# Performance work log

Hardware: AMD Instinct MI355X
Metric: run time of the kernel (lower is better)

Reference implementation:

```python
import jax, jax.numpy as jnp
import numpy as np

B, T, D = 2, 1024, 1024
U = 50257   # units (vocab)
S = 8192    # negatives sampled


def setup_inputs() -> dict:
    key = jax.random.key(0)
    k1, k2, k3, k4, k5 = jax.random.split(key, 5)
    logits = jax.random.normal(k1, (B, T, D), dtype=jnp.float32)
    kernel = jax.random.normal(k2, (U, D), dtype=jnp.float32) * 0.02
    bias = jax.random.normal(k3, (U,), dtype=jnp.float32) * 0.01
    targets = jax.random.randint(k4, (B, T), 0, U, dtype=jnp.int32)
    sampled = jax.random.randint(k5, (S,), 0, U, dtype=jnp.int32)
    return {"logits": logits, "kernel": kernel, "bias": bias,
            "targets": targets, "sampled": sampled}


def _log_uniform_logq(ids, num_classes):
    # log of log-uniform (Zipfian) sampling probability, as in
    # tf.random.log_uniform_candidate_sampler
    idf = ids.astype(jnp.float32)
    return jnp.log(jnp.log1p(1.0 / (idf + 1.0)) / jnp.log(float(num_classes + 1)))


def reference(logits, kernel, bias, targets, sampled):
    num_classes = kernel.shape[0]
    num_sampled = sampled.shape[0]
    x = logits.reshape(-1, logits.shape[-1])      # [N, D]
    t = targets.reshape(-1)                        # [N]

    # Full-softmax output probabilities (layer's returned tensor)
    full_logits = x @ kernel.T + bias              # [N, U]
    probs = jax.nn.softmax(full_logits, axis=-1)

    # Sampled softmax training loss (tf.nn.sampled_softmax_loss math)
    log_s = jnp.log(jnp.float32(num_sampled))
    true_w = kernel[t]                             # [N, D] gather
    true_b = bias[t]
    true_logits = jnp.sum(x * true_w, axis=-1) + true_b \
        - (log_s + _log_uniform_logq(t, num_classes))          # [N]

    samp_w = kernel[sampled]                       # [S, D] gather
    samp_b = bias[sampled]
    samp_logits = x @ samp_w.T + samp_b \
        - (log_s + _log_uniform_logq(sampled, num_classes))    # [N, S]

    # remove accidental hits: sampled negative equals the true class
    acc = t[:, None] == sampled[None, :]
    samp_logits = jnp.where(acc, jnp.float32(-1e9), samp_logits)

    all_logits = jnp.concatenate([true_logits[:, None], samp_logits], axis=1)
    # cross entropy with label index 0 (the true class slot)
    per_token = jax.nn.logsumexp(all_logits, axis=1) - all_logits[:, 0]
    loss = jnp.mean(per_token)  # weights all ones -> SUM_OVER_BATCH_SIZE

    return probs.reshape(targets.shape + (num_classes,)), loss
```

## Files before the change

### kernel.cpp

```cpp
#include <hip/hip_runtime.h>
#include <hip/hip_bf16.h>
#include <stdint.h>

#define N_ROWS 2048
#define DK 1024
#define NU 50257
#define NS 8192

typedef __bf16 bf16x8 __attribute__((ext_vector_type(8)));
typedef float f32x4 __attribute__((ext_vector_type(4)));
typedef float vf4 __attribute__((ext_vector_type(4)));
typedef unsigned vu2 __attribute__((ext_vector_type(2)));
typedef unsigned vu4 __attribute__((ext_vector_type(4)));

__device__ __forceinline__ unsigned short f2bf_rne(float f) {
  union { float f; unsigned u; } v; v.f = f;
  unsigned u = v.u;
  return (unsigned short)((u + 0x7FFFu + ((u >> 16) & 1u)) >> 16);
}
__device__ __forceinline__ unsigned pack2(float lo, float hi) {
  return (unsigned)f2bf_rne(lo) | ((unsigned)f2bf_rne(hi) << 16);
}

__global__ void cvt_f32_bf16(const float* __restrict__ in,
                             unsigned short* __restrict__ out, unsigned n) {
  unsigned i = (blockIdx.x * 256u + threadIdx.x) * 8u;
  if (i >= n) return;
  const vf4* p = (const vf4*)(in + i);
  vf4 a = __builtin_nontemporal_load(p);
  vf4 b = __builtin_nontemporal_load(p + 1);
  vu4 o;
  o.x = pack2(a.x, a.y); o.y = pack2(a.z, a.w);
  o.z = pack2(b.x, b.y); o.w = pack2(b.z, b.w);
  *(vu4*)(out + i) = o;
}

__global__ void gather_sampled(const float* __restrict__ kern,
                               const float* __restrict__ bias,
                               const int* __restrict__ sampled,
                               unsigned short* __restrict__ sw,
                               float* __restrict__ adj) {
  int j = blockIdx.x;
  int s = sampled[j];
  const float* src = kern + (size_t)s * DK;
  unsigned short* dst = sw + (size_t)j * DK;
  int c = threadIdx.x * 4;
  vf4 v = __builtin_nontemporal_load((const vf4*)(src + c));
  vu2 o; o.x = pack2(v.x, v.y); o.y = pack2(v.z, v.w);
  *(vu2*)(dst + c) = o;
  if (threadIdx.x == 0) {
    float lq = logf(log1pf(1.0f / ((float)s + 1.0f))) - logf(logf((float)(NU + 1)));
    adj[j] = bias[s] - (logf((float)NS) + lq);
  }
}

__global__ void true_logits_k(const float* __restrict__ x, const float* __restrict__ kern,
                              const float* __restrict__ bias, const int* __restrict__ targets,
                              float* __restrict__ true_logit, float* __restrict__ loss_acc) {
  int row = blockIdx.x * 4 + (threadIdx.x >> 6);
  int lane = threadIdx.x & 63;
  int t = targets[row];
  const float* xr = x + (size_t)row * DK;
  const float* wr = kern + (size_t)t * DK;
  float s = 0.f;
  #pragma unroll
  for (int it = 0; it < 4; ++it) {
    int c = lane * 4 + it * 256;
    float4 a = *(const float4*)(xr + c);
    float4 b = *(const float4*)(wr + c);
    s += a.x * b.x + a.y * b.y + a.z * b.z + a.w * b.w;
  }
  #pragma unroll
  for (int off = 32; off > 0; off >>= 1) s += __shfl_xor(s, off, 64);
  if (lane == 0) {
    float lq = logf(log1pf(1.0f / ((float)t + 1.0f))) - logf(logf((float)(NU + 1)));
    float tl = s + bias[t] - (logf((float)NS) + lq);
    true_logit[row] = tl;
    atomicAdd(&loss_acc[row], __expf(tl));
  }
}

__global__ __launch_bounds__(256) void gemm_probs(
    const unsigned short* __restrict__ A,
    const unsigned short* __restrict__ Bm,
    const float* __restrict__ bias,
    float* __restrict__ out, float* __restrict__ row_sum) {
  __shared__ alignas(16) unsigned char smem[32 * 132 * 4];
  unsigned short* As = (unsigned short*)smem;
  unsigned short* Bs = (unsigned short*)(smem + 8192);
  float* ot = (float*)smem;

  const int tid = threadIdx.x;
  const int wave = tid >> 6, lane = tid & 63;
  const int bid = blockIdx.x;
  const int sb = (bid & 7) * 786 + (bid >> 3);
  const int rb = (sb & 15) << 7;
  const int cb = (sb >> 4) << 7;
  const int wm = wave & 1, wn = wave >> 1;
  const int q = lane >> 4, l15 = lane & 15;
  const int srow = lane >> 2, scol = lane & 3;

  f32x4 acc[4][4] = {};

  const int seg0 = wave * 2;
  const unsigned short* ga0 = A + (size_t)(rb + seg0 * 16 + srow) * DK + scol * 8;
  const unsigned short* ga1 = ga0 + (size_t)16 * DK;
  int bu0 = cb + seg0 * 16 + srow;       if (bu0 > NU - 1) bu0 = NU - 1;
  int bu1 = cb + (seg0 + 1) * 16 + srow; if (bu1 > NU - 1) bu1 = NU - 1;
  const unsigned short* gb0 = Bm + (size_t)bu0 * DK + scol * 8;
  const unsigned short* gb1 = Bm + (size_t)bu1 * DK + scol * 8;
  unsigned short* la0 = As + (seg0) * 512;
  unsigned short* la1 = As + (seg0 + 1) * 512;
  unsigned short* lb0 = Bs + (seg0) * 512;
  unsigned short* lb1 = Bs + (seg0 + 1) * 512;

  for (int kb = 0; kb < DK; kb += 32) {
    __builtin_amdgcn_global_load_lds((__attribute__((address_space(1))) void*)(ga0 + kb),
                                     (__attribute__((address_space(3))) void*)la0, 16, 0, 0);
    __builtin_amdgcn_global_load_lds((__attribute__((address_space(1))) void*)(ga1 + kb),
                                     (__attribute__((address_space(3))) void*)la1, 16, 0, 0);
    __builtin_amdgcn_global_load_lds((__attribute__((address_space(1))) void*)(gb0 + kb),
                                     (__attribute__((address_space(3))) void*)lb0, 16, 0, 0);
    __builtin_amdgcn_global_load_lds((__attribute__((address_space(1))) void*)(gb1 + kb),
                                     (__attribute__((address_space(3))) void*)lb1, 16, 0, 0);
    __syncthreads();
    bf16x8 af[4], bfr[4];
    #pragma unroll
    for (int mi = 0; mi < 4; ++mi)
      af[mi] = *(const bf16x8*)&As[(wm * 64 + mi * 16 + l15) * 32 + q * 8];
    #pragma unroll
    for (int ni = 0; ni < 4; ++ni)
      bfr[ni] = *(const bf16x8*)&Bs[(wn * 64 + ni * 16 + l15) * 32 + q * 8];
    #pragma unroll
    for (int mi = 0; mi < 4; ++mi)
      #pragma unroll
      for (int ni = 0; ni < 4; ++ni)
        acc[mi][ni] = __builtin_amdgcn_mfma_f32_16x16x32_bf16(af[mi], bfr[ni], acc[mi][ni], 0, 0, 0);
    __syncthreads();
  }

  const bool full_panel = (cb + 128 <= NU);
  #pragma unroll
  for (int mi = 0; mi < 4; ++mi) {
    #pragma unroll
    for (int ni = 0; ni < 4; ++ni) {
      int col = cb + wn * 64 + ni * 16 + l15;
      int bcol = col < NU ? col : NU - 1;
      float bv = bias[bcol];
      f32x4 c = acc[mi][ni];
      #pragma unroll
      for (int r = 0; r < 4; ++r)
        ot[(wm * 16 + q * 4 + r) * 132 + wn * 64 + ni * 16 + l15] = __expf(c[r] + bv);
    }
    __syncthreads();
    {
      int lr = tid >> 3;
      int sub = tid & 7;
      int grow = rb + (lr >> 4) * 64 + mi * 16 + (lr & 15);
      float* gout = out + (size_t)grow * NU + cb;
      const float* lrow = ot + lr * 132;
      float sum = 0.f;
      if (full_panel) {
        #pragma unroll
        for (int p = 0; p < 4; ++p) {
          int c = p * 32 + sub * 4;
          vf4 v = *(const vf4*)(lrow + c);
          sum += v.x + v.y + v.z + v.w;
          __builtin_nontemporal_store(v, (vf4*)(gout + c));
        }
      } else {
        #pragma unroll
        for (int p = 0; p < 4; ++p) {
          int c = p * 32 + sub * 4;
          #pragma unroll
          for (int e = 0; e < 4; ++e) {
            if (cb + c + e < NU) {
              float v = lrow[c + e];
              sum += v;
              __builtin_nontemporal_store(v, gout + c + e);
            }
          }
        }
      }
      sum += __shfl_xor(sum, 1, 64);
      sum += __shfl_xor(sum, 2, 64);
      sum += __shfl_xor(sum, 4, 64);
      if (sub == 0) atomicAdd(&row_sum[grow], sum);
    }
    __syncthreads();
  }
}

__global__ __launch_bounds__(256) void gemm_sampled(
    const unsigned short* __restrict__ A, const unsigned short* __restrict__ SW,
    const float* __restrict__ adj, const int* __restrict__ sampled,
    const int* __restrict__ targets, float* __restrict__ loss_acc) {
  __shared__ alignas(16) unsigned short As[128 * 32];
  __shared__ alignas(16) unsigned short Bs[128 * 32];
  const int tid = threadIdx.x;
  const int wave = tid >> 6, lane = tid & 63;
  const int bid = blockIdx.x;
  const int sb = (bid & 7) * 128 + (bid >> 3);
  const int rb = (sb & 15) << 7;
  const int cb = (sb >> 4) << 7;
  const int wm = wave & 1, wn = wave >> 1;
  const int q = lane >> 4, l15 = lane & 15;
  const int srow = lane >> 2, scol = lane & 3;

  f32x4 acc[4][4] = {};

  const int seg0 = wave * 2;
  const unsigned short* ga0 = A + (size_t)(rb + seg0 * 16 + srow) * DK + scol * 8;
  const unsigned short* ga1 = ga0 + (size_t)16 * DK;
  const unsigned short* gb0 = SW + (size_t)(cb + seg0 * 16 + srow) * DK + scol * 8;
  const unsigned short* gb1 = gb0 + (size_t)16 * DK;
  unsigned short* la0 = &As[(seg0) * 512];
  unsigned short* la1 = &As[(seg0 + 1) * 512];
  unsigned short* lb0 = &Bs[(seg0) * 512];
  unsigned short* lb1 = &Bs[(seg0 + 1) * 512];

  for (int kb = 0; kb < DK; kb += 32) {
    __builtin_amdgcn_global_load_lds((__attribute__((address_space(1))) void*)(ga0 + kb),
                                     (__attribute__((address_space(3))) void*)la0, 16, 0, 0);
    __builtin_amdgcn_global_load_lds((__attribute__((address_space(1))) void*)(ga1 + kb),
                                     (__attribute__((address_space(3))) void*)la1, 16, 0, 0);
    __builtin_amdgcn_global_load_lds((__attribute__((address_space(1))) void*)(gb0 + kb),
                                     (__attribute__((address_space(3))) void*)lb0, 16, 0, 0);
    __builtin_amdgcn_global_load_lds((__attribute__((address_space(1))) void*)(gb1 + kb),
                                     (__attribute__((address_space(3))) void*)lb1, 16, 0, 0);
    __syncthreads();
    bf16x8 af[4], bfr[4];
    #pragma unroll
    for (int mi = 0; mi < 4; ++mi)
      af[mi] = *(const bf16x8*)&As[(wm * 64 + mi * 16 + l15) * 32 + q * 8];
    #pragma unroll
    for (int ni = 0; ni < 4; ++ni)
      bfr[ni] = *(const bf16x8*)&Bs[(wn * 64 + ni * 16 + l15) * 32 + q * 8];
    #pragma unroll
    for (int mi = 0; mi < 4; ++mi)
      #pragma unroll
      for (int ni = 0; ni < 4; ++ni)
        acc[mi][ni] = __builtin_amdgcn_mfma_f32_16x16x32_bf16(af[mi], bfr[ni], acc[mi][ni], 0, 0, 0);
    __syncthreads();
  }

  #pragma unroll
  for (int mi = 0; mi < 4; ++mi) {
    int row0 = rb + wm * 64 + mi * 16 + q * 4;
    int t0 = targets[row0], t1 = targets[row0 + 1], t2 = targets[row0 + 2], t3 = targets[row0 + 3];
    float rs[4] = {0.f, 0.f, 0.f, 0.f};
    #pragma unroll
    for (int ni = 0; ni < 4; ++ni) {
      int col = cb + wn * 64 + ni * 16 + l15;
      float av = adj[col];
      int sid = sampled[col];
      f32x4 c = acc[mi][ni];
      rs[0] += (sid == t0) ? 0.f : __expf(c[0] + av);
      rs[1] += (sid == t1) ? 0.f : __expf(c[1] + av);
      rs[2] += (sid == t2) ? 0.f : __expf(c[2] + av);
      rs[3] += (sid == t3) ? 0.f : __expf(c[3] + av);
    }
    #pragma unroll
    for (int r = 0; r < 4; ++r) {
      float v = rs[r];
      v += __shfl_xor(v, 1, 64);
      v += __shfl_xor(v, 2, 64);
      v += __shfl_xor(v, 4, 64);
      v += __shfl_xor(v, 8, 64);
      if (l15 == 0) atomicAdd(&loss_acc[row0 + r], v);
    }
  }
}

__global__ void prep_inv(const float* __restrict__ row_sum, float* __restrict__ inv) {
  int i = blockIdx.x * 256 + threadIdx.x;
  if (i < N_ROWS) inv[i] = 1.0f / row_sum[i];
}

__global__ void scale_probs(float* __restrict__ out, const float* __restrict__ inv, unsigned n4) {
  unsigned i = blockIdx.x * 256u + threadIdx.x;
  if (i >= n4) return;
  constexpr unsigned long long MAGIC = ((1ull << 45) + 50256ull) / 50257ull;
  vf4 v = __builtin_nontemporal_load((const vf4*)out + i);
  unsigned long long base = (unsigned long long)i * 4ull;
  unsigned r0 = (unsigned)((base * MAGIC) >> 45);
  unsigned r1 = (unsigned)(((base + 1) * MAGIC) >> 45);
  unsigned r2 = (unsigned)(((base + 2) * MAGIC) >> 45);
  unsigned r3 = (unsigned)(((base + 3) * MAGIC) >> 45);
  v.x *= inv[r0]; v.y *= inv[r1]; v.z *= inv[r2]; v.w *= inv[r3];
  __builtin_nontemporal_store(v, (vf4*)out + i);
}

__global__ void finalize_loss(const float* __restrict__ loss_acc,
                              const float* __restrict__ true_logit,
                              float* __restrict__ loss_out) {
  __shared__ float red[256];
  float s = 0.f;
  for (int i = threadIdx.x; i < N_ROWS; i += 256)
    s += logf(loss_acc[i]) - true_logit[i];
  red[threadIdx.x] = s;
  __syncthreads();
  for (int off = 128; off > 0; off >>= 1) {
    if (threadIdx.x < off) red[threadIdx.x] += red[threadIdx.x + off];
    __syncthreads();
  }
  if (threadIdx.x == 0) loss_out[0] = red[0] / (float)N_ROWS;
}

extern "C" void kernel_launch(void* const* d_in, const int* in_sizes, int n_in,
                              void* d_out, int out_size, void* d_ws, size_t ws_size,
                              hipStream_t stream) {
  const float* x = (const float*)d_in[0];
  const float* kern = (const float*)d_in[1];
  const float* bias = (const float*)d_in[2];
  const int* targets = (const int*)d_in[3];
  const int* sampled = (const int*)d_in[4];
  float* out = (float*)d_out;

  char* ws = (char*)d_ws;
  size_t off = 0;
  unsigned short* kbf = (unsigned short*)(ws + off); off += (size_t)NU * DK * 2;
  unsigned short* xbf = (unsigned short*)(ws + off); off += (size_t)N_ROWS * DK * 2;
  unsigned short* swbf = (unsigned short*)(ws + off); off += (size_t)NS * DK * 2;
  float* adj = (float*)(ws + off); off += (size_t)NS * 4;
  float* row_sum = (float*)(ws + off); off += (size_t)N_ROWS * 4;
  float* inv_rs = (float*)(ws + off); off += (size_t)N_ROWS * 4;
  float* loss_acc = (float*)(ws + off); off += (size_t)N_ROWS * 4;
  float* true_l = (float*)(ws + off); off += (size_t)N_ROWS * 4;

  hipMemsetAsync(row_sum, 0, N_ROWS * 4, stream);
  hipMemsetAsync(loss_acc, 0, N_ROWS * 4, stream);

  {
    unsigned n = NU * DK;
    cvt_f32_bf16<<<(n / 8 + 255) / 256, 256, 0, stream>>>(kern, kbf, n);
  }
  {
    unsigned n = N_ROWS * DK;
    cvt_f32_bf16<<<(n / 8 + 255) / 256, 256, 0, stream>>>(x, xbf, n);
  }
  gather_sampled<<<NS, 256, 0, stream>>>(kern, bias, sampled, swbf, adj);
  true_logits_k<<<N_ROWS / 4, 256, 0, stream>>>(x, kern, bias, targets, true_l, loss_acc);

  gemm_probs<<<dim3(6288), 256, 0, stream>>>(xbf, kbf, bias, out, row_sum);

  gemm_sampled<<<dim3(1024), 256, 0, stream>>>(xbf, swbf, adj, sampled, targets, loss_acc);

  prep_inv<<<(N_ROWS + 255) / 256, 256, 0, stream>>>(row_sum, inv_rs);

  {
    unsigned n4 = (unsigned)(((size_t)N_ROWS * NU) / 4);
    scale_probs<<<(n4 + 255u) / 256u, 256, 0, stream>>>(out, inv_rs, n4);
  }
  finalize_loss<<<1, 256, 0, stream>>>(loss_acc, true_l, out + (size_t)N_ROWS * NU);
}
```

Measured before the change: 1.031 ms.

## Gather sampled rows from bf16 kernel in-GEMM, align prob stores, row-wise scaling

```diff
diff --git a/kernel.cpp b/kernel.cpp
--- a/kernel.cpp
+++ b/kernel.cpp
@@ -35,20 +35,12 @@
   *(vu4*)(out + i) = o;
 }
 
-__global__ void gather_sampled(const float* __restrict__ kern,
-                               const float* __restrict__ bias,
-                               const int* __restrict__ sampled,
-                               unsigned short* __restrict__ sw,
-                               float* __restrict__ adj) {
-  int j = blockIdx.x;
-  int s = sampled[j];
-  const float* src = kern + (size_t)s * DK;
-  unsigned short* dst = sw + (size_t)j * DK;
-  int c = threadIdx.x * 4;
-  vf4 v = __builtin_nontemporal_load((const vf4*)(src + c));
-  vu2 o; o.x = pack2(v.x, v.y); o.y = pack2(v.z, v.w);
-  *(vu2*)(dst + c) = o;
-  if (threadIdx.x == 0) {
+__global__ void compute_adj(const float* __restrict__ bias,
+                            const int* __restrict__ sampled,
+                            float* __restrict__ adj) {
+  int j = blockIdx.x * 256 + threadIdx.x;
+  if (j < NS) {
+    int s = sampled[j];
     float lq = logf(log1pf(1.0f / ((float)s + 1.0f))) - logf(logf((float)(NU + 1)));
     adj[j] = bias[s] - (logf((float)NS) + lq);
   }
@@ -157,16 +149,64 @@
       int lr = tid >> 3;
       int sub = tid & 7;
       int grow = rb + (lr >> 4) * 64 + mi * 16 + (lr & 15);
-      float* gout = out + (size_t)grow * NU + cb;
+      size_t base = (size_t)grow * NU + cb;
+      float* gout = out + base;
       const float* lrow = ot + lr * 132;
       float sum = 0.f;
       if (full_panel) {
-        #pragma unroll
-        for (int p = 0; p < 4; ++p) {
-          int c = p * 32 + sub * 4;
-          vf4 v = *(const vf4*)(lrow + c);
-          sum += v.x + v.y + v.z + v.w;
-          __builtin_nontemporal_store(v, (vf4*)(gout + c));
+        int c0 = sub * 16;
+        vf4 v0 = *(const vf4*)(lrow + c0);
+        vf4 v1 = *(const vf4*)(lrow + c0 + 4);
+        vf4 v2 = *(const vf4*)(lrow + c0 + 8);
+        vf4 v3 = *(const vf4*)(lrow + c0 + 12);
+        sum = v0.x + v0.y + v0.z + v0.w + v1.x + v1.y + v1.z + v1.w
+            + v2.x + v2.y + v2.z + v2.w + v3.x + v3.y + v3.z + v3.w;
+        float* g = gout + c0;
+        int mis = (int)((4 - (base & 3)) & 3);
+        vf4 t;
+        switch (mis) {
+          case 0:
+            __builtin_nontemporal_store(v0, (vf4*)g);
+            __builtin_nontemporal_store(v1, (vf4*)(g + 4));
+            __builtin_nontemporal_store(v2, (vf4*)(g + 8));
+            __builtin_nontemporal_store(v3, (vf4*)(g + 12));
+            break;
+          case 1:
+            __builtin_nontemporal_store(v0.x, g);
+            t.x = v0.y; t.y = v0.z; t.z = v0.w; t.w = v1.x;
+            __builtin_nontemporal_store(t, (vf4*)(g + 1));
+            t.x = v1.y; t.y = v1.z; t.z = v1.w; t.w = v2.x;
+            __builtin_nontemporal_store(t, (vf4*)(g + 5));
+            t.x = v2.y; t.y = v2.z; t.z = v2.w; t.w = v3.x;
+            __builtin_nontemporal_store(t, (vf4*)(g + 9));
+            __builtin_nontemporal_store(v3.y, g + 13);
+            __builtin_nontemporal_store(v3.z, g + 14);
+            __builtin_nontemporal_store(v3.w, g + 15);
+            break;
+          case 2:
+            __builtin_nontemporal_store(v0.x, g);
+            __builtin_nontemporal_store(v0.y, g + 1);
+            t.x = v0.z; t.y = v0.w; t.z = v1.x; t.w = v1.y;
+            __builtin_nontemporal_store(t, (vf4*)(g + 2));
+            t.x = v1.z; t.y = v1.w; t.z = v2.x; t.w = v2.y;
+            __builtin_nontemporal_store(t, (vf4*)(g + 6));
+            t.x = v2.z; t.y = v2.w; t.z = v3.x; t.w = v3.y;
+            __builtin_nontemporal_store(t, (vf4*)(g + 10));
+            __builtin_nontemporal_store(v3.z, g + 14);
+            __builtin_nontemporal_store(v3.w, g + 15);
+            break;
+          default:
+            __builtin_nontemporal_store(v0.x, g);
+            __builtin_nontemporal_store(v0.y, g + 1);
+            __builtin_nontemporal_store(v0.z, g + 2);
+            t.x = v0.w; t.y = v1.x; t.z = v1.y; t.w = v1.z;
+            __builtin_nontemporal_store(t, (vf4*)(g + 3));
+            t.x = v1.w; t.y = v2.x; t.z = v2.y; t.w = v2.z;
+            __builtin_nontemporal_store(t, (vf4*)(g + 7));
+            t.x = v2.w; t.y = v3.x; t.z = v3.y; t.w = v3.z;
+            __builtin_nontemporal_store(t, (vf4*)(g + 11));
+            __builtin_nontemporal_store(v3.w, g + 15);
+            break;
         }
       } else {
         #pragma unroll
@@ -192,7 +232,7 @@
 }
 
 __global__ __launch_bounds__(256) void gemm_sampled(
-    const unsigned short* __restrict__ A, const unsigned short* __restrict__ SW,
+    const unsigned short* __restrict__ A, const unsigned short* __restrict__ Kb,
     const float* __restrict__ adj, const int* __restrict__ sampled,
     const int* __restrict__ targets, float* __restrict__ loss_acc) {
   __shared__ alignas(16) unsigned short As[128 * 32];
@@ -212,8 +252,10 @@
   const int seg0 = wave * 2;
   const unsigned short* ga0 = A + (size_t)(rb + seg0 * 16 + srow) * DK + scol * 8;
   const unsigned short* ga1 = ga0 + (size_t)16 * DK;
-  const unsigned short* gb0 = SW + (size_t)(cb + seg0 * 16 + srow) * DK + scol * 8;
-  const unsigned short* gb1 = gb0 + (size_t)16 * DK;
+  int s0 = sampled[cb + seg0 * 16 + srow];
+  int s1 = sampled[cb + (seg0 + 1) * 16 + srow];
+  const unsigned short* gb0 = Kb + (size_t)s0 * DK + scol * 8;
+  const unsigned short* gb1 = Kb + (size_t)s1 * DK + scol * 8;
   unsigned short* la0 = &As[(seg0) * 512];
   unsigned short* la1 = &As[(seg0 + 1) * 512];
   unsigned short* lb0 = &Bs[(seg0) * 512];
@@ -272,23 +314,25 @@
   }
 }
 
-__global__ void prep_inv(const float* __restrict__ row_sum, float* __restrict__ inv) {
-  int i = blockIdx.x * 256 + threadIdx.x;
-  if (i < N_ROWS) inv[i] = 1.0f / row_sum[i];
-}
-
-__global__ void scale_probs(float* __restrict__ out, const float* __restrict__ inv, unsigned n4) {
-  unsigned i = blockIdx.x * 256u + threadIdx.x;
-  if (i >= n4) return;
-  constexpr unsigned long long MAGIC = ((1ull << 45) + 50256ull) / 50257ull;
-  vf4 v = __builtin_nontemporal_load((const vf4*)out + i);
-  unsigned long long base = (unsigned long long)i * 4ull;
-  unsigned r0 = (unsigned)((base * MAGIC) >> 45);
-  unsigned r1 = (unsigned)(((base + 1) * MAGIC) >> 45);
-  unsigned r2 = (unsigned)(((base + 2) * MAGIC) >> 45);
-  unsigned r3 = (unsigned)(((base + 3) * MAGIC) >> 45);
-  v.x *= inv[r0]; v.y *= inv[r1]; v.z *= inv[r2]; v.w *= inv[r3];
-  __builtin_nontemporal_store(v, (vf4*)out + i);
+__global__ __launch_bounds__(256) void scale_probs_rows(float* __restrict__ out,
+                                                        const float* __restrict__ row_sum) {
+  int row = blockIdx.x;
+  size_t base = (size_t)row * NU;
+  float inv = 1.0f / row_sum[row];
+  float* p = out + base;
+  int mis = (int)((4 - (base & 3)) & 3);
+  int t = threadIdx.x;
+  if (t < mis) p[t] *= inv;
+  int nb = (NU - mis) >> 2;
+  for (int j = t; j < nb; j += 256) {
+    vf4* q = (vf4*)(p + mis + 4 * j);
+    vf4 v = __builtin_nontemporal_load(q);
+    v.x *= inv; v.y *= inv; v.z *= inv; v.w *= inv;
+    __builtin_nontemporal_store(v, q);
+  }
+  int done = mis + 4 * nb;
+  int rem = NU - done;
+  if (t < rem) p[done + t] *= inv;
 }
 
 __global__ void finalize_loss(const float* __restrict__ loss_acc,
@@ -321,10 +365,8 @@
   size_t off = 0;
   unsigned short* kbf = (unsigned short*)(ws + off); off += (size_t)NU * DK * 2;
   unsigned short* xbf = (unsigned short*)(ws + off); off += (size_t)N_ROWS * DK * 2;
-  unsigned short* swbf = (unsigned short*)(ws + off); off += (size_t)NS * DK * 2;
   float* adj = (float*)(ws + off); off += (size_t)NS * 4;
   float* row_sum = (float*)(ws + off); off += (size_t)N_ROWS * 4;
-  float* inv_rs = (float*)(ws + off); off += (size_t)N_ROWS * 4;
   float* loss_acc = (float*)(ws + off); off += (size_t)N_ROWS * 4;
   float* true_l = (float*)(ws + off); off += (size_t)N_ROWS * 4;
 
@@ -339,18 +381,14 @@
     unsigned n = N_ROWS * DK;
     cvt_f32_bf16<<<(n / 8 + 255) / 256, 256, 0, stream>>>(x, xbf, n);
   }
-  gather_sampled<<<NS, 256, 0, stream>>>(kern, bias, sampled, swbf, adj);
+  compute_adj<<<(NS + 255) / 256, 256, 0, stream>>>(bias, sampled, adj);
   true_logits_k<<<N_ROWS / 4, 256, 0, stream>>>(x, kern, bias, targets, true_l, loss_acc);
 
   gemm_probs<<<dim3(6288), 256, 0, stream>>>(xbf, kbf, bias, out, row_sum);
 
-  gemm_sampled<<<dim3(1024), 256, 0, stream>>>(xbf, swbf, adj, sampled, targets, loss_acc);
-
-  prep_inv<<<(N_ROWS + 255) / 256, 256, 0, stream>>>(row_sum, inv_rs);
-
-  {
-    unsigned n4 = (unsigned)(((size_t)N_ROWS * NU) / 4);
-    scale_probs<<<(n4 + 255u) / 256u, 256, 0, stream>>>(out, inv_rs, n4);
-  }
+  gemm_sampled<<<dim3(1024), 256, 0, stream>>>(xbf, kbf, adj, sampled, targets, loss_acc);
+
+  scale_probs_rows<<<N_ROWS, 256, 0, stream>>>(out, row_sum);
+
   finalize_loss<<<1, 256, 0, stream>>>(loss_acc, true_l, out + (size_t)N_ROWS * NU);
 }
```

Result: slower. 1.144 ms (+10.9%).

## Replace row-sum atomics with per-panel partials and row-wise scaling pass

Applied to the files above, without the earlier changes.

```diff
diff --git a/kernel.cpp b/kernel.cpp
--- a/kernel.cpp
+++ b/kernel.cpp
@@ -6,6 +6,7 @@
 #define DK 1024
 #define NU 50257
 #define NS 8192
+#define NPAN 393
 
 typedef __bf16 bf16x8 __attribute__((ext_vector_type(8)));
 typedef float f32x4 __attribute__((ext_vector_type(4)));
@@ -84,7 +85,7 @@
     const unsigned short* __restrict__ A,
     const unsigned short* __restrict__ Bm,
     const float* __restrict__ bias,
-    float* __restrict__ out, float* __restrict__ row_sum) {
+    float* __restrict__ out, float* __restrict__ part) {
   __shared__ alignas(16) unsigned char smem[32 * 132 * 4];
   unsigned short* As = (unsigned short*)smem;
   unsigned short* Bs = (unsigned short*)(smem + 8192);
@@ -95,7 +96,8 @@
   const int bid = blockIdx.x;
   const int sb = (bid & 7) * 786 + (bid >> 3);
   const int rb = (sb & 15) << 7;
-  const int cb = (sb >> 4) << 7;
+  const int panel = sb >> 4;
+  const int cb = panel << 7;
   const int wm = wave & 1, wn = wave >> 1;
   const int q = lane >> 4, l15 = lane & 15;
   const int srow = lane >> 2, scol = lane & 3;
@@ -166,7 +168,7 @@
           int c = p * 32 + sub * 4;
           vf4 v = *(const vf4*)(lrow + c);
           sum += v.x + v.y + v.z + v.w;
-          __builtin_nontemporal_store(v, (vf4*)(gout + c));
+          __builtin_memcpy(gout + c, &v, 16);
         }
       } else {
         #pragma unroll
@@ -177,7 +179,7 @@
             if (cb + c + e < NU) {
               float v = lrow[c + e];
               sum += v;
-              __builtin_nontemporal_store(v, gout + c + e);
+              gout[c + e] = v;
             }
           }
         }
@@ -185,7 +187,7 @@
       sum += __shfl_xor(sum, 1, 64);
       sum += __shfl_xor(sum, 2, 64);
       sum += __shfl_xor(sum, 4, 64);
-      if (sub == 0) atomicAdd(&row_sum[grow], sum);
+      if (sub == 0) part[(size_t)grow * NPAN + panel] = sum;
     }
     __syncthreads();
   }
@@ -272,23 +274,38 @@
   }
 }
 
-__global__ void prep_inv(const float* __restrict__ row_sum, float* __restrict__ inv) {
-  int i = blockIdx.x * 256 + threadIdx.x;
-  if (i < N_ROWS) inv[i] = 1.0f / row_sum[i];
-}
-
-__global__ void scale_probs(float* __restrict__ out, const float* __restrict__ inv, unsigned n4) {
-  unsigned i = blockIdx.x * 256u + threadIdx.x;
-  if (i >= n4) return;
-  constexpr unsigned long long MAGIC = ((1ull << 45) + 50256ull) / 50257ull;
-  vf4 v = __builtin_nontemporal_load((const vf4*)out + i);
-  unsigned long long base = (unsigned long long)i * 4ull;
-  unsigned r0 = (unsigned)((base * MAGIC) >> 45);
-  unsigned r1 = (unsigned)(((base + 1) * MAGIC) >> 45);
-  unsigned r2 = (unsigned)(((base + 2) * MAGIC) >> 45);
-  unsigned r3 = (unsigned)(((base + 3) * MAGIC) >> 45);
-  v.x *= inv[r0]; v.y *= inv[r1]; v.z *= inv[r2]; v.w *= inv[r3];
-  __builtin_nontemporal_store(v, (vf4*)out + i);
+__global__ void reduce_inv(const float* __restrict__ part, float* __restrict__ inv) {
+  int row = blockIdx.x;
+  const float* pr = part + (size_t)row * NPAN;
+  float s = 0.f;
+  for (int i = threadIdx.x; i < NPAN; i += 64) s += pr[i];
+  #pragma unroll
+  for (int off = 32; off > 0; off >>= 1) s += __shfl_xor(s, off, 64);
+  if (threadIdx.x == 0) inv[row] = 1.0f / s;
+}
+
+__global__ __launch_bounds__(256) void scale_probs2(float* __restrict__ out,
+                                                    const float* __restrict__ inv_rs) {
+  int row = blockIdx.y;
+  size_t base = (size_t)row * NU;
+  float inv = inv_rs[row];
+  float* p = out + base;
+  int mis = (int)((4 - (base & 3)) & 3);
+  int t = threadIdx.x;
+  if (blockIdx.x == 0 && t < mis) p[t] *= inv;
+  int start = mis + blockIdx.x * 4096;
+  #pragma unroll
+  for (int u = 0; u < 4; ++u) {
+    int j = start + t * 4 + u * 1024;
+    if (j + 4 <= NU) {
+      vf4* q = (vf4*)(p + j);
+      vf4 v = __builtin_nontemporal_load(q);
+      v.x *= inv; v.y *= inv; v.z *= inv; v.w *= inv;
+      __builtin_nontemporal_store(v, q);
+    } else if (j < NU) {
+      for (int e = 0; e < NU - j; ++e) p[j + e] *= inv;
+    }
+  }
 }
 
 __global__ void finalize_loss(const float* __restrict__ loss_acc,
@@ -323,12 +340,11 @@
   unsigned short* xbf = (unsigned short*)(ws + off); off += (size_t)N_ROWS * DK * 2;
   unsigned short* swbf = (unsigned short*)(ws + off); off += (size_t)NS * DK * 2;
   float* adj = (float*)(ws + off); off += (size_t)NS * 4;
-  float* row_sum = (float*)(ws + off); off += (size_t)N_ROWS * 4;
+  float* part = (float*)(ws + off); off += (size_t)N_ROWS * NPAN * 4;
   float* inv_rs = (float*)(ws + off); off += (size_t)N_ROWS * 4;
   float* loss_acc = (float*)(ws + off); off += (size_t)N_ROWS * 4;
   float* true_l = (float*)(ws + off); off += (size_t)N_ROWS * 4;
 
-  hipMemsetAsync(row_sum, 0, N_ROWS * 4, stream);
   hipMemsetAsync(loss_acc, 0, N_ROWS * 4, stream);
 
   {
@@ -342,15 +358,13 @@
   gather_sampled<<<NS, 256, 0, stream>>>(kern, bias, sampled, swbf, adj);
   true_logits_k<<<N_ROWS / 4, 256, 0, stream>>>(x, kern, bias, targets, true_l, loss_acc);
 
-  gemm_probs<<<dim3(6288), 256, 0, stream>>>(xbf, kbf, bias, out, row_sum);
+  gemm_probs<<<dim3(6288), 256, 0, stream>>>(xbf, kbf, bias, out, part);
 
   gemm_sampled<<<dim3(1024), 256, 0, stream>>>(xbf, swbf, adj, sampled, targets, loss_acc);
 
-  prep_inv<<<(N_ROWS + 255) / 256, 256, 0, stream>>>(row_sum, inv_rs);
-
-  {
-    unsigned n4 = (unsigned)(((size_t)N_ROWS * NU) / 4);
-    scale_probs<<<(n4 + 255u) / 256u, 256, 0, stream>>>(out, inv_rs, n4);
-  }
+  reduce_inv<<<N_ROWS, 64, 0, stream>>>(part, inv_rs);
+
+  scale_probs2<<<dim3(13, N_ROWS), 256, 0, stream>>>(out, inv_rs);
+
   finalize_loss<<<1, 256, 0, stream>>>(loss_acc, true_l, out + (size_t)N_ROWS * NU);
 }
```

After: 1.055 ms. 1.02x slower.
